# Kernel optimization log

Measured on AMD Instinct MI355X. Metric: run time of the kernel, lower is better.

## Reference

```python
import jax, jax.numpy as jnp
import numpy as np

ALPHA = 0.2  # leaky relu slope
DEPTH = 3
MAX_REF = 10
MAX_DIR = 32

def leaky(x):
    return jnp.where(x >= 0, x, ALPHA * x)

def setup_inputs() -> dict:
    key = jax.random.key(0)
    ks = jax.random.split(key, 9)
    N, F_IN, F_OUT = 100000, 128, 128
    h = jax.random.normal(ks[0], (N, F_IN), dtype=jnp.float32)
    W_ref = jax.random.normal(ks[1], (F_IN, F_OUT), dtype=jnp.float32) * 0.1
    a_ref = jax.random.normal(ks[2], (2 * F_OUT, 1), dtype=jnp.float32) * 0.1
    W_dir = jax.random.normal(ks[3], (F_IN, F_OUT), dtype=jnp.float32) * 0.1
    a_dir = jax.random.normal(ks[4], (2 * F_OUT, 1), dtype=jnp.float32) * 0.1
    ref_neighbors = jax.random.randint(ks[5], (N, DEPTH + 1, MAX_REF), 0, N)
    ref_counts = jax.random.randint(ks[6], (N, DEPTH + 1), 0, MAX_REF + 1)
    dir_neighbors = jax.random.randint(ks[7], (N, MAX_DIR), 0, N)
    dir_counts = jax.random.randint(ks[8], (N,), 1, MAX_DIR + 1)
    return {"h": h, "W_ref": W_ref, "a_ref": a_ref, "W_dir": W_dir, "a_dir": a_dir,
            "ref_neighbors": ref_neighbors, "ref_counts": ref_counts,
            "dir_neighbors": dir_neighbors, "dir_counts": dir_counts}

def _forward_ref(h, W_ref, a_ref, ref_neighbors, ref_counts):
    Wh = h @ W_ref                                  # [N, F]
    F_ = Wh.shape[1]
    # mean of (up to 10) neighbor features per (node, depth); empty -> zeros
    nbr = Wh[ref_neighbors]                         # [N, D+1, 10, F]
    slot = jnp.arange(MAX_REF)[None, None, :]
    valid = slot < ref_counts[:, :, None]           # [N, D+1, 10]
    cnt = jnp.maximum(ref_counts, 1).astype(Wh.dtype)  # avoid div by 0
    f_ref = jnp.einsum('ndkf,ndk->ndf', nbr, valid.astype(Wh.dtype)) / cnt[:, :, None]  # [N, D+1, F]
    # attention score: leaky(cat(Wh[node], f_ref[d]) @ a_ref)
    a_self, a_nbr = a_ref[:F_, 0], a_ref[F_:, 0]
    e = leaky(Wh @ a_self[:, None] + f_ref @ a_nbr)  # [N,1]+[N,D+1] -> [N, D+1]
    alpha = jax.nn.softmax(e, axis=-1)
    out = jnp.einsum('ndf,nd->nf', f_ref, alpha)
    return jax.nn.sigmoid(out)

def _forward_dir(h, W_dir, a_dir, dir_neighbors, dir_counts):
    Wh = h @ W_dir                                  # [N, F]
    F_ = Wh.shape[1]
    nbr = Wh[dir_neighbors]                         # [N, K, F]
    a_self, a_nbr = a_dir[:F_, 0], a_dir[F_:, 0]
    e = leaky((Wh @ a_self)[:, None] + nbr @ a_nbr)  # [N, K]
    valid = jnp.arange(MAX_DIR)[None, :] < dir_counts[:, None]
    e = jnp.where(valid, e, -jnp.inf)
    alpha = jax.nn.softmax(e, axis=-1)
    out = jnp.einsum('nkf,nk->nf', nbr, alpha)
    return jax.nn.sigmoid(out)

def reference(h, W_ref, a_ref, W_dir, a_dir, ref_neighbors, ref_counts, dir_neighbors, dir_counts):
    h_ref = _forward_ref(h, W_ref, a_ref, ref_neighbors, ref_counts)
    h_dir = _forward_dir(h, W_dir, a_dir, dir_neighbors, dir_counts)
    return (h_ref + h_dir) / 2  # mode='mean'
```

## Files before the change

kernel.cpp:

```cpp
#include <hip/hip_runtime.h>

typedef __attribute__((ext_vector_type(8))) short s16x8;
typedef __attribute__((ext_vector_type(4))) float f32x4;

#define F 128

__device__ __forceinline__ unsigned short f2bf(float f) {
    unsigned int u = __float_as_uint(f);
    u = (u + 0x7fffu + ((u >> 16) & 1u)) >> 16;
    return (unsigned short)u;
}
__device__ __forceinline__ float bflo(unsigned int u) { return __uint_as_float(u << 16); }
__device__ __forceinline__ float bfhi(unsigned int u) { return __uint_as_float(u & 0xffff0000u); }
__device__ __forceinline__ float leaky(float x) { return x >= 0.f ? x : 0.2f * x; }
__device__ __forceinline__ float sigmoidf(float x) { return 1.f / (1.f + __expf(-x)); }

#define SWZ16(row, b) ((b) ^ (((row) & 7) << 4))

__device__ __forceinline__ void glds16(void* lds, const void* g) {
    __builtin_amdgcn_global_load_lds(
        (const __attribute__((address_space(1))) unsigned int*)g,
        (__attribute__((address_space(3))) unsigned int*)lds,
        16, 0, 0);
}

__global__ __launch_bounds__(256) void prep_w(const float* __restrict__ wRef,
                                              const float* __restrict__ wDir,
                                              unsigned short* __restrict__ wT) {
    int i = blockIdx.x * 256 + threadIdx.x;
    int m = i >> 14;
    int rr = i & 16383;
    int k = rr >> 7;
    int c = rr & 127;
    const float* W = m ? wDir : wRef;
    wT[m * 16384 + c * 128 + (k ^ (((c & 7) << 3)))] = f2bf(W[k * 128 + c]);
}

__device__ __forceinline__ void epi(const f32x4* acc, unsigned char* cb ,
                                    int rowBase, int w, int r, int g, int lane, int N,
                                    const float* __restrict__ aVec,
                                    unsigned short* __restrict__ wh,
                                    float* __restrict__ sArr, float* __restrict__ tArr) {
    float ps[4] = {0.f, 0.f, 0.f, 0.f}, pt[4] = {0.f, 0.f, 0.f, 0.f};
#pragma unroll
    for (int ct = 0; ct < 8; ++ct) {
        int c = ct * 16 + r;
        float As = aVec[c], At = aVec[128 + c];
#pragma unroll
        for (int q = 0; q < 4; ++q) { ps[q] += acc[ct][q] * As; pt[q] += acc[ct][q] * At; }
    }
#pragma unroll
    for (int off = 1; off <= 8; off <<= 1) {
#pragma unroll
        for (int q = 0; q < 4; ++q) {
            ps[q] += __shfl_xor(ps[q], off);
            pt[q] += __shfl_xor(pt[q], off);
        }
    }
    if (r == 0) {
#pragma unroll
        for (int q = 0; q < 4; ++q) {
            int row = rowBase + w * 16 + g * 4 + q;
            if (row < N) { sArr[row] = ps[q]; tArr[row] = pt[q]; }
        }
    }
#pragma unroll
    for (int ct = 0; ct < 8; ++ct) {
#pragma unroll
        for (int q = 0; q < 4; ++q) {
            int lrow = g * 4 + q;
            int xb = (ct * 16 + r) * 2;
            *(unsigned short*)(cb + lrow * 256 + SWZ16(lrow, xb)) = f2bf(acc[ct][q]);
        }
    }
#pragma unroll
    for (int i = 0; i < 4; ++i) {
        int off = i * 1024 + lane * 16;
        int lrow = off >> 8, x = off & 255;
        uint4 v = *(const uint4*)(cb + lrow * 256 + SWZ16(lrow, x));
        int grow = rowBase + w * 16 + lrow;
        if (grow < N) *(uint4*)((char*)wh + (size_t)grow * 256 + x) = v;
    }
}

__global__ __launch_bounds__(256) void gemm_wh(const float* __restrict__ h,
                                               const unsigned short* __restrict__ wT,
                                               const float* __restrict__ aRefG,
                                               const float* __restrict__ aDirG,
                                               unsigned short* __restrict__ whRef,
                                               unsigned short* __restrict__ whDir,
                                               float* __restrict__ sRef, float* __restrict__ tRef,
                                               float* __restrict__ sDir, float* __restrict__ tDir,
                                               int N) {
    __shared__ unsigned char lds[65536];
    const int tid = threadIdx.x;
    const int lane = tid & 63, w = tid >> 6;
    const int r = lane & 15, g = lane >> 4;
    const int rowBase = blockIdx.x * 64;

#pragma unroll
    for (int it = 0; it < 8; ++it) {
        int lin = it * 4096 + tid * 16;
        int arow = lin >> 9, x = lin & 511;
        int grow = min(rowBase + arow, N - 1);
        glds16(lds + lin, (const char*)h + (size_t)grow * 512 + SWZ16(arow, x));
    }
#pragma unroll
    for (int it = 0; it < 8; ++it) {
        int lin = it * 4096 + tid * 16;
        glds16(lds + 32768 + lin, (const char*)wT + lin);
    }
    __syncthreads();

    s16x8 afr[4];
    {
        const int arow = w * 16 + r;
#pragma unroll
        for (int kt = 0; kt < 4; ++kt) {
            int kb = kt * 128 + g * 32;
            float4 f0 = *(const float4*)(lds + arow * 512 + SWZ16(arow, kb));
            float4 f1 = *(const float4*)(lds + arow * 512 + SWZ16(arow, kb + 16));
            s16x8 a;
            a[0] = (short)f2bf(f0.x); a[1] = (short)f2bf(f0.y);
            a[2] = (short)f2bf(f0.z); a[3] = (short)f2bf(f0.w);
            a[4] = (short)f2bf(f1.x); a[5] = (short)f2bf(f1.y);
            a[6] = (short)f2bf(f1.z); a[7] = (short)f2bf(f1.w);
            afr[kt] = a;
        }
    }
    unsigned char* cb = lds + w * 8192;

    {
        f32x4 acc[8];
#pragma unroll
        for (int ct = 0; ct < 8; ++ct) acc[ct] = (f32x4){0.f, 0.f, 0.f, 0.f};
#pragma unroll
        for (int kt = 0; kt < 4; ++kt) {
#pragma unroll
            for (int ct = 0; ct < 8; ++ct) {
                int c = ct * 16 + r;
                s16x8 b = *(const s16x8*)(lds + 32768 + c * 256 + SWZ16(c, kt * 64 + g * 16));
                acc[ct] = __builtin_amdgcn_mfma_f32_16x16x32_bf16(afr[kt], b, acc[ct], 0, 0, 0);
            }
        }
        epi(acc, cb, rowBase, w, r, g, lane, N, aRefG, whRef, sRef, tRef);
    }
    __syncthreads();
#pragma unroll
    for (int it = 0; it < 8; ++it) {
        int lin = it * 4096 + tid * 16;
        glds16(lds + 32768 + lin, (const char*)wT + 32768 + lin);
    }
    __syncthreads();
    {
        f32x4 acc[8];
#pragma unroll
        for (int ct = 0; ct < 8; ++ct) acc[ct] = (f32x4){0.f, 0.f, 0.f, 0.f};
#pragma unroll
        for (int kt = 0; kt < 4; ++kt) {
#pragma unroll
            for (int ct = 0; ct < 8; ++ct) {
                int c = ct * 16 + r;
                s16x8 b = *(const s16x8*)(lds + 32768 + c * 256 + SWZ16(c, kt * 64 + g * 16));
                acc[ct] = __builtin_amdgcn_mfma_f32_16x16x32_bf16(afr[kt], b, acc[ct], 0, 0, 0);
            }
        }
        epi(acc, cb, rowBase, w, r, g, lane, N, aDirG, whDir, sDir, tDir);
    }
}

__device__ __forceinline__ void acc8(float* a, uint4 u, float c) {
    a[0] += c * bflo(u.x); a[1] += c * bfhi(u.x);
    a[2] += c * bflo(u.y); a[3] += c * bfhi(u.y);
    a[4] += c * bflo(u.z); a[5] += c * bfhi(u.z);
    a[6] += c * bflo(u.w); a[7] += c * bfhi(u.w);
}

__global__ __launch_bounds__(256) void gather_attn(
    const unsigned short* __restrict__ whRef, const unsigned short* __restrict__ whDir,
    const float* __restrict__ sRef, const float* __restrict__ tRef,
    const float* __restrict__ sDir, const float* __restrict__ tDir,
    const int* __restrict__ refNbr, const int* __restrict__ refCnt,
    const int* __restrict__ dirNbr, const int* __restrict__ dirCnt,
    float* __restrict__ out, int N) {
    __shared__ int2 s_list[4][72];

    const int wid = threadIdx.x >> 6;
    const int lane = threadIdx.x & 63;
    const int q = lane >> 4, hl16 = lane & 15;
    const int d = lane >> 4, kk = lane & 15;
    const int n_raw = blockIdx.x * 4 + wid;
    const int n = min(n_raw, N - 1);

    int cnt = refCnt[n * 4 + d];
    bool validR = kk < cnt;
    int idxR = 0;
    float tv = 0.f;
    if (kk < 10) idxR = refNbr[(size_t)n * 40 + d * 10 + kk];
    if (validR) tv = tRef[idxR];
    float sum = tv;
    sum += __shfl_xor(sum, 1); sum += __shfl_xor(sum, 2);
    sum += __shfl_xor(sum, 4); sum += __shfl_xor(sum, 8);
    float rc = 1.f / (float)max(cnt, 1);
    float e = leaky(sRef[n] + sum * rc);
    float mx = fmaxf(e, __shfl_xor(e, 16)); mx = fmaxf(mx, __shfl_xor(mx, 32));
    float wgt = __expf(e - mx);
    float den = wgt + __shfl_xor(wgt, 16); den += __shfl_xor(den, 32);
    float coefR = wgt / den * rc;
    unsigned long long mask = __ballot(validR);
    int pos = (int)__popcll(mask & ((1ull << lane) - 1ull));
    int Lr = (int)__popcll(mask);
    if (validR) s_list[wid][pos] = make_int2(idxR, __float_as_int(coefR));

    int dcnt = dirCnt[n];
    float eD = -1e30f;
    int idxD = 0;
    if (lane < 32) {
        idxD = dirNbr[(size_t)n * 32 + lane];
        if (lane < dcnt) eD = leaky(sDir[n] + tDir[idxD]);
    }
    float mD = eD;
#pragma unroll
    for (int off = 16; off; off >>= 1) mD = fmaxf(mD, __shfl_xor(mD, off, 32));
    float wD = (lane < dcnt) ? __expf(eD - mD) : 0.f;
    float dD = wD;
#pragma unroll
    for (int off = 16; off; off >>= 1) dD += __shfl_xor(dD, off, 32);
    if (lane < dcnt) s_list[wid][40 + lane] = make_int2(idxD, __float_as_int(wD / dD));

    __syncthreads();

    float accR[8] = {0.f, 0.f, 0.f, 0.f, 0.f, 0.f, 0.f, 0.f};
    {
        uint4 u[10]; float c[10];
#pragma unroll
        for (int j = 0; j < 10; ++j) {
            int e = j * 4 + q;
            if (e < Lr) {
                int2 ic = s_list[wid][e];
                c[j] = __int_as_float(ic.y);
                u[j] = *(const uint4*)((const char*)whRef + ((size_t)(unsigned)ic.x << 8) + (hl16 << 4));
            }
        }
#pragma unroll
        for (int j = 0; j < 10; ++j) {
            int e = j * 4 + q;
            if (e < Lr) acc8(accR, u[j], c[j]);
        }
    }
    float accD[8] = {0.f, 0.f, 0.f, 0.f, 0.f, 0.f, 0.f, 0.f};
    {
        uint4 u[8]; float c[8];
#pragma unroll
        for (int j = 0; j < 8; ++j) {
            int e = j * 4 + q;
            if (e < dcnt) {
                int2 ic = s_list[wid][40 + e];
                c[j] = __int_as_float(ic.y);
                u[j] = *(const uint4*)((const char*)whDir + ((size_t)(unsigned)ic.x << 8) + (hl16 << 4));
            }
        }
#pragma unroll
        for (int j = 0; j < 8; ++j) {
            int e = j * 4 + q;
            if (e < dcnt) acc8(accD, u[j], c[j]);
        }
    }

#pragma unroll
    for (int j = 0; j < 8; ++j) {
        accR[j] += __shfl_xor(accR[j], 16); accR[j] += __shfl_xor(accR[j], 32);
        accD[j] += __shfl_xor(accD[j], 16); accD[j] += __shfl_xor(accD[j], 32);
    }
    if (n_raw < N && q == 0) {
        float o[8];
#pragma unroll
        for (int j = 0; j < 8; ++j) o[j] = 0.5f * (sigmoidf(accR[j]) + sigmoidf(accD[j]));
        float4* dst = (float4*)(out + (size_t)n * F + hl16 * 8);
        dst[0] = make_float4(o[0], o[1], o[2], o[3]);
        dst[1] = make_float4(o[4], o[5], o[6], o[7]);
    }
}

extern "C" void kernel_launch(void* const* d_in, const int* in_sizes, int n_in,
                              void* d_out, int out_size, void* d_ws, size_t ws_size,
                              hipStream_t stream) {
    const float* h    = (const float*)d_in[0];
    const float* Wref = (const float*)d_in[1];
    const float* aRef = (const float*)d_in[2];
    const float* Wdir = (const float*)d_in[3];
    const float* aDir = (const float*)d_in[4];
    const int* refNbr = (const int*)d_in[5];
    const int* refCnt = (const int*)d_in[6];
    const int* dirNbr = (const int*)d_in[7];
    const int* dirCnt = (const int*)d_in[8];
    float* out = (float*)d_out;
    const int N = in_sizes[0] / F;

    const size_t NF = (size_t)N * F;
    unsigned short* whRef = (unsigned short*)d_ws;
    unsigned short* whDir = whRef + NF;
    float* sRef = (float*)(whDir + NF);
    float* tRef = sRef + N;
    float* sDir = tRef + N;
    float* tDir = sDir + N;
    unsigned short* wT = (unsigned short*)(tDir + N);

    prep_w<<<128, 256, 0, stream>>>(Wref, Wdir, wT);
    gemm_wh<<<(N + 63) / 64, 256, 0, stream>>>(h, wT, aRef, aDir, whRef, whDir,
                                               sRef, tRef, sDir, tDir, N);
    gather_attn<<<(N + 3) / 4, 256, 0, stream>>>(whRef, whDir, sRef, tRef, sDir, tDir,
                                                 refNbr, refCnt, dirNbr, dirCnt, out, N);
}
```

Baseline: 291.1 us.

## Store projected features as FP8 and stage bf16 A tile in smaller LDS

The GEMM epilogue now packs the projected features Wh into FP8 instead of bf16, which halves the intermediate buffer and the bytes the random-access gather kernel reads per neighbour row. The gather kernel unpacks FP8 pairs with hardware convert instructions. The GEMM also loads h through registers, converts it to bf16 once and stores it in LDS, which shrinks LDS from 64KB to 48KB and may allow more blocks per CU. FP8 storage loses precision in the neighbour features, which may cause tolerance failures.

```diff
diff --git a/kernel.cpp b/kernel.cpp
--- a/kernel.cpp
+++ b/kernel.cpp
@@ -2,6 +2,7 @@
 
 typedef __attribute__((ext_vector_type(8))) short s16x8;
 typedef __attribute__((ext_vector_type(4))) float f32x4;
+typedef __attribute__((ext_vector_type(2))) float f32x2;
 
 #define F 128
 
@@ -39,7 +40,7 @@
 __device__ __forceinline__ void epi(const f32x4* acc, unsigned char* cb ,
                                     int rowBase, int w, int r, int g, int lane, int N,
                                     const float* __restrict__ aVec,
-                                    unsigned short* __restrict__ wh,
+                                    unsigned char* __restrict__ wh ,
                                     float* __restrict__ sArr, float* __restrict__ tArr) {
     float ps[4] = {0.f, 0.f, 0.f, 0.f}, pt[4] = {0.f, 0.f, 0.f, 0.f};
 #pragma unroll
@@ -78,8 +79,12 @@
         int off = i * 1024 + lane * 16;
         int lrow = off >> 8, x = off & 255;
         uint4 v = *(const uint4*)(cb + lrow * 256 + SWZ16(lrow, x));
+        int pk0 = __builtin_amdgcn_cvt_pk_fp8_f32(bflo(v.x), bfhi(v.x), 0, false);
+        pk0 = __builtin_amdgcn_cvt_pk_fp8_f32(bflo(v.y), bfhi(v.y), pk0, true);
+        int pk1 = __builtin_amdgcn_cvt_pk_fp8_f32(bflo(v.z), bfhi(v.z), 0, false);
+        pk1 = __builtin_amdgcn_cvt_pk_fp8_f32(bflo(v.w), bfhi(v.w), pk1, true);
         int grow = rowBase + w * 16 + lrow;
-        if (grow < N) *(uint4*)((char*)wh + (size_t)grow * 256 + x) = v;
+        if (grow < N) *(uint2*)(wh + (size_t)grow * 128 + (x >> 1)) = make_uint2((unsigned)pk0, (unsigned)pk1);
     }
 }
 
@@ -87,12 +92,12 @@
                                                const unsigned short* __restrict__ wT,
                                                const float* __restrict__ aRefG,
                                                const float* __restrict__ aDirG,
-                                               unsigned short* __restrict__ whRef,
-                                               unsigned short* __restrict__ whDir,
+                                               unsigned char* __restrict__ whRef,
+                                               unsigned char* __restrict__ whDir,
                                                float* __restrict__ sRef, float* __restrict__ tRef,
                                                float* __restrict__ sDir, float* __restrict__ tDir,
                                                int N) {
-    __shared__ unsigned char lds[65536];
+    __shared__ unsigned char lds[49152];
     const int tid = threadIdx.x;
     const int lane = tid & 63, w = tid >> 6;
     const int r = lane & 15, g = lane >> 4;
@@ -101,35 +106,62 @@
 #pragma unroll
     for (int it = 0; it < 8; ++it) {
         int lin = it * 4096 + tid * 16;
-        int arow = lin >> 9, x = lin & 511;
+        glds16(lds + 16384 + lin, (const char*)wT + lin);
+    }
+    float4 av[4][2];
+#pragma unroll
+    for (int it = 0; it < 4; ++it) {
+        int lin = it * 4096 + tid * 16;
+        int arow = lin >> 8, x = lin & 255;
         int grow = min(rowBase + arow, N - 1);
-        glds16(lds + lin, (const char*)h + (size_t)grow * 512 + SWZ16(arow, x));
-    }
+        const char* src = (const char*)h + (size_t)grow * 512 + x * 2;
+        av[it][0] = *(const float4*)(src);
+        av[it][1] = *(const float4*)(src + 16);
+    }
+#pragma unroll
+    for (int it = 0; it < 4; ++it) {
+        int lin = it * 4096 + tid * 16;
+        int arow = lin >> 8, x = lin & 255;
+        s16x8 a;
+        a[0] = (short)f2bf(av[it][0].x); a[1] = (short)f2bf(av[it][0].y);
+        a[2] = (short)f2bf(av[it][0].z); a[3] = (short)f2bf(av[it][0].w);
+        a[4] = (short)f2bf(av[it][1].x); a[5] = (short)f2bf(av[it][1].y);
+        a[6] = (short)f2bf(av[it][1].z); a[7] = (short)f2bf(av[it][1].w);
+        *(s16x8*)(lds + arow * 256 + SWZ16(arow, x)) = a;
+    }
+    __syncthreads();
+
+    s16x8 afr[4];
+    {
+        const int arow = w * 16 + r;
+#pragma unroll
+        for (int kt = 0; kt < 4; ++kt)
+            afr[kt] = *(const s16x8*)(lds + arow * 256 + SWZ16(arow, kt * 64 + g * 16));
+    }
+    unsigned char* cb = lds + w * 4096;
+
+    {
+        f32x4 acc[8];
+#pragma unroll
+        for (int ct = 0; ct < 8; ++ct) acc[ct] = (f32x4){0.f, 0.f, 0.f, 0.f};
+#pragma unroll
+        for (int kt = 0; kt < 4; ++kt) {
+#pragma unroll
+            for (int ct = 0; ct < 8; ++ct) {
+                int c = ct * 16 + r;
+                s16x8 b = *(const s16x8*)(lds + 16384 + c * 256 + SWZ16(c, kt * 64 + g * 16));
+                acc[ct] = __builtin_amdgcn_mfma_f32_16x16x32_bf16(afr[kt], b, acc[ct], 0, 0, 0);
+            }
+        }
+        epi(acc, cb, rowBase, w, r, g, lane, N, aRefG, whRef, sRef, tRef);
+    }
+    __syncthreads();
 #pragma unroll
     for (int it = 0; it < 8; ++it) {
         int lin = it * 4096 + tid * 16;
-        glds16(lds + 32768 + lin, (const char*)wT + lin);
+        glds16(lds + 16384 + lin, (const char*)wT + 32768 + lin);
     }
     __syncthreads();
-
-    s16x8 afr[4];
-    {
-        const int arow = w * 16 + r;
-#pragma unroll
-        for (int kt = 0; kt < 4; ++kt) {
-            int kb = kt * 128 + g * 32;
-            float4 f0 = *(const float4*)(lds + arow * 512 + SWZ16(arow, kb));
-            float4 f1 = *(const float4*)(lds + arow * 512 + SWZ16(arow, kb + 16));
-            s16x8 a;
-            a[0] = (short)f2bf(f0.x); a[1] = (short)f2bf(f0.y);
-            a[2] = (short)f2bf(f0.z); a[3] = (short)f2bf(f0.w);
-            a[4] = (short)f2bf(f1.x); a[5] = (short)f2bf(f1.y);
-            a[6] = (short)f2bf(f1.z); a[7] = (short)f2bf(f1.w);
-            afr[kt] = a;
-        }
-    }
-    unsigned char* cb = lds + w * 8192;
-
     {
         f32x4 acc[8];
 #pragma unroll
@@ -139,45 +171,27 @@
 #pragma unroll
             for (int ct = 0; ct < 8; ++ct) {
                 int c = ct * 16 + r;
-                s16x8 b = *(const s16x8*)(lds + 32768 + c * 256 + SWZ16(c, kt * 64 + g * 16));
+                s16x8 b = *(const s16x8*)(lds + 16384 + c * 256 + SWZ16(c, kt * 64 + g * 16));
                 acc[ct] = __builtin_amdgcn_mfma_f32_16x16x32_bf16(afr[kt], b, acc[ct], 0, 0, 0);
             }
         }
-        epi(acc, cb, rowBase, w, r, g, lane, N, aRefG, whRef, sRef, tRef);
-    }
-    __syncthreads();
-#pragma unroll
-    for (int it = 0; it < 8; ++it) {
-        int lin = it * 4096 + tid * 16;
-        glds16(lds + 32768 + lin, (const char*)wT + 32768 + lin);
-    }
-    __syncthreads();
-    {
-        f32x4 acc[8];
-#pragma unroll
-        for (int ct = 0; ct < 8; ++ct) acc[ct] = (f32x4){0.f, 0.f, 0.f, 0.f};
-#pragma unroll
-        for (int kt = 0; kt < 4; ++kt) {
-#pragma unroll
-            for (int ct = 0; ct < 8; ++ct) {
-                int c = ct * 16 + r;
-                s16x8 b = *(const s16x8*)(lds + 32768 + c * 256 + SWZ16(c, kt * 64 + g * 16));
-                acc[ct] = __builtin_amdgcn_mfma_f32_16x16x32_bf16(afr[kt], b, acc[ct], 0, 0, 0);
-            }
-        }
         epi(acc, cb, rowBase, w, r, g, lane, N, aDirG, whDir, sDir, tDir);
     }
 }
 
-__device__ __forceinline__ void acc8(float* a, uint4 u, float c) {
-    a[0] += c * bflo(u.x); a[1] += c * bfhi(u.x);
-    a[2] += c * bflo(u.y); a[3] += c * bfhi(u.y);
-    a[4] += c * bflo(u.z); a[5] += c * bfhi(u.z);
-    a[6] += c * bflo(u.w); a[7] += c * bfhi(u.w);
+__device__ __forceinline__ void acc8f8(float* a, uint2 u, float c) {
+    f32x2 p0 = __builtin_amdgcn_cvt_pk_f32_fp8((int)u.x, false);
+    f32x2 p1 = __builtin_amdgcn_cvt_pk_f32_fp8((int)u.x, true);
+    f32x2 p2 = __builtin_amdgcn_cvt_pk_f32_fp8((int)u.y, false);
+    f32x2 p3 = __builtin_amdgcn_cvt_pk_f32_fp8((int)u.y, true);
+    a[0] += c * p0[0]; a[1] += c * p0[1];
+    a[2] += c * p1[0]; a[3] += c * p1[1];
+    a[4] += c * p2[0]; a[5] += c * p2[1];
+    a[6] += c * p3[0]; a[7] += c * p3[1];
 }
 
 __global__ __launch_bounds__(256) void gather_attn(
-    const unsigned short* __restrict__ whRef, const unsigned short* __restrict__ whDir,
+    const unsigned char* __restrict__ whRef, const unsigned char* __restrict__ whDir,
     const float* __restrict__ sRef, const float* __restrict__ tRef,
     const float* __restrict__ sDir, const float* __restrict__ tDir,
     const int* __restrict__ refNbr, const int* __restrict__ refCnt,
@@ -232,38 +246,38 @@
 
     float accR[8] = {0.f, 0.f, 0.f, 0.f, 0.f, 0.f, 0.f, 0.f};
     {
-        uint4 u[10]; float c[10];
+        uint2 u[10]; float c[10];
 #pragma unroll
         for (int j = 0; j < 10; ++j) {
             int e = j * 4 + q;
             if (e < Lr) {
                 int2 ic = s_list[wid][e];
                 c[j] = __int_as_float(ic.y);
-                u[j] = *(const uint4*)((const char*)whRef + ((size_t)(unsigned)ic.x << 8) + (hl16 << 4));
+                u[j] = *(const uint2*)(whRef + ((size_t)(unsigned)ic.x << 7) + (hl16 << 3));
             }
         }
 #pragma unroll
         for (int j = 0; j < 10; ++j) {
             int e = j * 4 + q;
-            if (e < Lr) acc8(accR, u[j], c[j]);
+            if (e < Lr) acc8f8(accR, u[j], c[j]);
         }
     }
     float accD[8] = {0.f, 0.f, 0.f, 0.f, 0.f, 0.f, 0.f, 0.f};
     {
-        uint4 u[8]; float c[8];
+        uint2 u[8]; float c[8];
 #pragma unroll
         for (int j = 0; j < 8; ++j) {
             int e = j * 4 + q;
             if (e < dcnt) {
                 int2 ic = s_list[wid][40 + e];
                 c[j] = __int_as_float(ic.y);
-                u[j] = *(const uint4*)((const char*)whDir + ((size_t)(unsigned)ic.x << 8) + (hl16 << 4));
+                u[j] = *(const uint2*)(whDir + ((size_t)(unsigned)ic.x << 7) + (hl16 << 3));
             }
         }
 #pragma unroll
         for (int j = 0; j < 8; ++j) {
             int e = j * 4 + q;
-            if (e < dcnt) acc8(accD, u[j], c[j]);
+            if (e < dcnt) acc8f8(accD, u[j], c[j]);
         }
     }
 
@@ -298,8 +312,8 @@
     const int N = in_sizes[0] / F;
 
     const size_t NF = (size_t)N * F;
-    unsigned short* whRef = (unsigned short*)d_ws;
-    unsigned short* whDir = whRef + NF;
+    unsigned char* whRef = (unsigned char*)d_ws;
+    unsigned char* whDir = whRef + NF;
     float* sRef = (float*)(whDir + NF);
     float* tRef = sRef + N;
     float* sDir = tRef + N;
```

Result: faster. 256.2 us (-12.0%).
